# Kernel tuning notes

Hardware: AMD Instinct MI355X
Metric: run time of the kernel (lower is better)

The kernel has to match this reference:

```python
import jax, jax.numpy as jnp
import numpy as np

NEG_BIG = -9e15  # matches torch's -9000000000000000.0 masked-fill value
ALPHA = 0.2      # LeakyReLU negative slope


def setup_inputs() -> dict:
    key = jax.random.key(0)
    k1, k2, k3, k4 = jax.random.split(key, 4)
    N, F_in, F_out = 8192, 128, 64
    h = jax.random.normal(k1, (N, F_in), dtype=jnp.float32)
    adj = jax.random.randint(k2, (N, N), 0, 2).astype(jnp.float32)
    # Glorot(gain=1.414)-scale params
    W = jax.random.normal(k3, (F_in, F_out), dtype=jnp.float32) * (1.414 * np.sqrt(2.0 / (F_in + F_out)))
    a = jax.random.normal(k4, (2 * F_out, 1), dtype=jnp.float32) * (1.414 * np.sqrt(2.0 / (2 * F_out + 1)))
    return {"h": h, "adj": adj, "W": W, "a": a}


def reference(h, adj, W, a):
    F_out = W.shape[1]
    Wh = h @ W                               # [N, F_out]
    Wh1 = Wh @ a[:F_out, :]                  # [N, 1]
    Wh2 = Wh @ a[F_out:, :]                  # [N, 1]
    e = jax.nn.leaky_relu(Wh1 + Wh2.T, negative_slope=ALPHA)  # [N, N]
    attention = jnp.where(adj > 0, e, NEG_BIG)
    attention = jax.nn.softmax(attention, axis=1)
    # dropout omitted (eval mode / p applied only in training)
    h_prime = attention @ Wh                 # [N, F_out]
    return jax.nn.elu(h_prime)               # concat=True -> ELU
```

## Files before the change

### kernel.cpp

```cpp
#include <hip/hip_runtime.h>
#include <hip/hip_bf16.h>

#define N 8192
#define FIN 128
#define FOUT 64
#define ALPHA 0.2f
#define LOG2E 1.44269504f
#define JPW (N / 8)

typedef __attribute__((ext_vector_type(8))) short short8;
typedef __attribute__((ext_vector_type(4))) float f32x4;

static __device__ __forceinline__ unsigned fkey(float x) {
    unsigned u = __float_as_uint(x);
    return (u >> 31) ? ~u : (u | 0x80000000u);
}
static __device__ __forceinline__ float fdecode(unsigned k) {
    unsigned u = (k & 0x80000000u) ? (k & 0x7FFFFFFFu) : ~k;
    return __uint_as_float(u);
}

__global__ __launch_bounds__(256) void k_prep(const float* __restrict__ h,
                                              const float* __restrict__ W,
                                              const float* __restrict__ a,
                                              float* __restrict__ Wh,
                                              float* __restrict__ s,
                                              float* __restrict__ t,
                                              unsigned* __restrict__ keys) {
    __shared__ float lH[16 * FIN];
    __shared__ float lW[FIN * FOUT];
    __shared__ float red[8];
    const int tid = threadIdx.x;
    const int r0 = blockIdx.x * 16;
    {
        const float4* src = (const float4*)(h + (size_t)r0 * FIN);
        float4* dst = (float4*)lH;
        for (int i = tid; i < 16 * FIN / 4; i += 256) dst[i] = src[i];
        const float4* ws_ = (const float4*)W;
        float4* dw = (float4*)lW;
        for (int i = tid; i < FIN * FOUT / 4; i += 256) dw[i] = ws_[i];
    }
    __syncthreads();
    const int wave = tid >> 6, lane = tid & 63;
    float acc[4] = {0.f, 0.f, 0.f, 0.f};
    for (int k = 0; k < FIN; ++k) {
        float wv = lW[k * FOUT + lane];
#pragma unroll
        for (int r = 0; r < 4; ++r)
            acc[r] = fmaf(lH[(wave * 4 + r) * FIN + k], wv, acc[r]);
    }
    const float a1 = a[lane], a2 = a[FOUT + lane];
    float smx = -1e30f, tmx = -1e30f;
#pragma unroll
    for (int r = 0; r < 4; ++r) {
        int row = r0 + wave * 4 + r;
        Wh[(size_t)row * FOUT + lane] = acc[r];
        float sv = acc[r] * a1, tv = acc[r] * a2;
#pragma unroll
        for (int off = 32; off; off >>= 1) {
            sv += __shfl_xor(sv, off);
            tv += __shfl_xor(tv, off);
        }
        if (lane == 0) { s[row] = sv; t[row] = tv; }
        smx = fmaxf(smx, sv);
        tmx = fmaxf(tmx, tv);
    }
    if (lane == 0) { red[wave] = smx; red[4 + wave] = tmx; }
    __syncthreads();
    if (tid == 0) {
        float ms = fmaxf(fmaxf(red[0], red[1]), fmaxf(red[2], red[3]));
        float mt = fmaxf(fmaxf(red[4], red[5]), fmaxf(red[6], red[7]));
        atomicMax(keys + 0, fkey(ms));
        atomicMax(keys + 1, fkey(mt));
    }
}

__global__ __launch_bounds__(256) void k_pack(const float* __restrict__ Wh,
                                              __hip_bfloat16* __restrict__ WhB) {
    const int c = blockIdx.x;
    const int tn = threadIdx.x >> 6;
    const int lane = threadIdx.x & 63;
    const int quad = lane >> 4, l16 = lane & 15;
    const float* src = Wh + ((size_t)(c * 32 + quad * 8)) * FOUT + tn * 16 + l16;
    union { unsigned short u[8]; short8 v; } frag;
#pragma unroll
    for (int e = 0; e < 8; ++e) {
        __hip_bfloat16 b = __float2bfloat16(src[(size_t)e * FOUT]);
        frag.u[e] = *(unsigned short*)&b;
    }
    *(short8*)&WhB[(((size_t)c * 4 + tn) * 64 + lane) * 8] = frag.v;
}

__global__ __launch_bounds__(512, 4) void k_attn(const float* __restrict__ adj,
                                                 const __hip_bfloat16* __restrict__ WhB,
                                                 const float* __restrict__ s,
                                                 const float* __restrict__ t,
                                                 const unsigned* __restrict__ keys,
                                                 float* __restrict__ out) {
    __shared__ float shacc[8][4][64][4];
    __shared__ float shl[8][16];
    const int wave = threadIdx.x >> 6, lane = threadIdx.x & 63;
    const int quad = lane >> 4, l16 = lane & 15;
    const int i0 = blockIdx.x * 16;

    const float mraw = fdecode(keys[0]) + fdecode(keys[1]);
    const float mle = mraw > 0.f ? mraw : ALPHA * mraw;
    const float mm = mle * LOG2E;
    const float sm = s[i0 + l16];

    const float* arow = adj + (size_t)(i0 + l16) * N + wave * JPW + quad * 8;
    const float* trow = t + wave * JPW + quad * 8;
    const short8* BF = (const short8*)WhB;

    f32x4 acc0 = {0,0,0,0}, acc1 = {0,0,0,0}, acc2 = {0,0,0,0}, acc3 = {0,0,0,0};
    float lsum = 0.f;

    float4 ca0, ca1, ct0, ct1, na0, na1, nt0, nt1;
    ca0 = *(const float4*)(arow);     ca1 = *(const float4*)(arow + 4);
    ct0 = *(const float4*)(trow);     ct1 = *(const float4*)(trow + 4);

    const int UNITS = JPW / 32;
#pragma unroll 4
    for (int u = 0; u < UNITS; ++u) {
        if (u + 1 < UNITS) {
            const float* an = arow + (u + 1) * 32;
            const float* tn_ = trow + (u + 1) * 32;
            na0 = *(const float4*)(an);      na1 = *(const float4*)(an + 4);
            nt0 = *(const float4*)(tn_);     nt1 = *(const float4*)(tn_ + 4);
        }
        const size_t cidx = (size_t)(wave * UNITS + u) * 4;
        short8 b0 = BF[(cidx + 0) * 64 + lane];
        short8 b1 = BF[(cidx + 1) * 64 + lane];
        short8 b2 = BF[(cidx + 2) * 64 + lane];
        short8 b3 = BF[(cidx + 3) * 64 + lane];

        union { unsigned short u16[8]; short8 v; } af;
        const float* ap = (const float*)&ca0;
        const float* tp = (const float*)&ct0;
#pragma unroll
        for (int e = 0; e < 8; ++e) {
            float av = (e < 4) ? ap[e] : ((const float*)&ca1)[e - 4];
            float tv = (e < 4) ? tp[e] : ((const float*)&ct1)[e - 4];
            float x = sm + tv;
            float le = fmaxf(x, ALPHA * x);
            float ex = exp2f(fmaf(le, LOG2E, -mm));
            float p = av * ex;
            __hip_bfloat16 pb = __float2bfloat16(p);
            unsigned short ub = *(unsigned short*)&pb;
            af.u16[e] = ub;
            lsum += __uint_as_float(((unsigned)ub) << 16);
        }
        ca0 = na0; ca1 = na1; ct0 = nt0; ct1 = nt1;

        acc0 = __builtin_amdgcn_mfma_f32_16x16x32_bf16(af.v, b0, acc0, 0, 0, 0);
        acc1 = __builtin_amdgcn_mfma_f32_16x16x32_bf16(af.v, b1, acc1, 0, 0, 0);
        acc2 = __builtin_amdgcn_mfma_f32_16x16x32_bf16(af.v, b2, acc2, 0, 0, 0);
        acc3 = __builtin_amdgcn_mfma_f32_16x16x32_bf16(af.v, b3, acc3, 0, 0, 0);
    }

    lsum += __shfl_xor(lsum, 16);
    lsum += __shfl_xor(lsum, 32);

#pragma unroll
    for (int r = 0; r < 4; ++r) {
        shacc[wave][0][lane][r] = acc0[r];
        shacc[wave][1][lane][r] = acc1[r];
        shacc[wave][2][lane][r] = acc2[r];
        shacc[wave][3][lane][r] = acc3[r];
    }
    if (lane < 16) shl[wave][lane] = lsum;
    __syncthreads();

    if (wave == 4 && lane < 16) {
        float v = 0.f;
#pragma unroll
        for (int w = 0; w < 8; ++w) v += shl[w][lane];
        shl[0][lane] = v;
    }
    float tot[4] = {0.f, 0.f, 0.f, 0.f};
    if (wave < 4) {
#pragma unroll
        for (int w = 0; w < 8; ++w) {
            float4 c = *(const float4*)&shacc[w][wave][lane][0];
#pragma unroll
            for (int r = 0; r < 4; ++r) tot[r] += ((const float*)&c)[r];
        }
    }
    __syncthreads();
    if (wave < 4) {
#pragma unroll
        for (int r = 0; r < 4; ++r) {
            int row = quad * 4 + r;
            float l = shl[0][row];
            float v = tot[r] / l;
            float o = v > 0.f ? v : (exp2f(v * LOG2E) - 1.f);
            out[(size_t)(i0 + row) * FOUT + wave * 16 + l16] = o;
        }
    }
}

extern "C" void kernel_launch(void* const* d_in, const int* in_sizes, int n_in,
                              void* d_out, int out_size, void* d_ws, size_t ws_size,
                              hipStream_t stream) {
    const float* h   = (const float*)d_in[0];
    const float* adj = (const float*)d_in[1];
    const float* W   = (const float*)d_in[2];
    const float* a   = (const float*)d_in[3];
    float* out = (float*)d_out;

    float* Wh = (float*)d_ws;
    __hip_bfloat16* WhB = (__hip_bfloat16*)(Wh + (size_t)N * FOUT);
    float* s = (float*)(WhB + (size_t)N * FOUT);
    float* t = s + N;
    unsigned* keys = (unsigned*)(t + N);

    hipMemsetAsync(keys, 0, 2 * sizeof(unsigned), stream);
    k_prep<<<N / 16, 256, 0, stream>>>(h, W, a, Wh, s, t, keys);
    k_pack<<<N / 32, 256, 0, stream>>>(Wh, WhB);
    k_attn<<<N / 16, 512, 0, stream>>>(adj, WhB, s, t, keys, out);
}
```

Measured before the change: 427.1 us.

## Stage adjacency tiles through LDS with async global-to-LDS double buffering

Restructures the attention kernel so the block streams 256-column slabs of the adjacency rows and t into double-buffered LDS via global_load_lds, with a barrier per stage. Waves are now split into 4 output-column tiles by 2 column halves, so each wave keeps one MFMA accumulator instead of four, and the final cross-wave reduction shrinks. The exp/leaky-relu work is now repeated by the four column-tile waves (4x redundant transcendental work per element) in exchange for coalesced, asynchronous loads and lower register pressure. The occupancy hint in launch bounds is dropped and a barrier is added per stage.

```diff
diff --git a/kernel.cpp b/kernel.cpp
--- a/kernel.cpp
+++ b/kernel.cpp
@@ -6,7 +6,9 @@
 #define FOUT 64
 #define ALPHA 0.2f
 #define LOG2E 1.44269504f
-#define JPW (N / 8)
+#define STJ 256
+#define NSTAGES (N / STJ)
+#define RS 260
 
 typedef __attribute__((ext_vector_type(8))) short short8;
 typedef __attribute__((ext_vector_type(4))) float f32x4;
@@ -18,6 +20,12 @@
 static __device__ __forceinline__ float fdecode(unsigned k) {
     unsigned u = (k & 0x80000000u) ? (k & 0x7FFFFFFFu) : ~k;
     return __uint_as_float(u);
+}
+
+static __device__ __forceinline__ void gll16(const float* g, float* l) {
+    __builtin_amdgcn_global_load_lds(
+        (const __attribute__((address_space(1))) unsigned int*)g,
+        (__attribute__((address_space(3))) unsigned int*)l, 16, 0, 0);
 }
 
 __global__ __launch_bounds__(256) void k_prep(const float* __restrict__ h,
@@ -91,108 +99,94 @@
     *(short8*)&WhB[(((size_t)c * 4 + tn) * 64 + lane) * 8] = frag.v;
 }
 
-__global__ __launch_bounds__(512, 4) void k_attn(const float* __restrict__ adj,
-                                                 const __hip_bfloat16* __restrict__ WhB,
-                                                 const float* __restrict__ s,
-                                                 const float* __restrict__ t,
-                                                 const unsigned* __restrict__ keys,
-                                                 float* __restrict__ out) {
-    __shared__ float shacc[8][4][64][4];
-    __shared__ float shl[8][16];
+__global__ __launch_bounds__(512) void k_attn(const float* __restrict__ adj,
+                                              const __hip_bfloat16* __restrict__ WhB,
+                                              const float* __restrict__ s,
+                                              const float* __restrict__ t,
+                                              const unsigned* __restrict__ keys,
+                                              float* __restrict__ out) {
+    __shared__ float bufA[2][16 * RS];
+    __shared__ float bufT[2][STJ];
+    __shared__ float shacc[8][64][4];
+    __shared__ float shl[2][16];
     const int wave = threadIdx.x >> 6, lane = threadIdx.x & 63;
     const int quad = lane >> 4, l16 = lane & 15;
+    const int ct = wave & 3, jh = wave >> 2;
     const int i0 = blockIdx.x * 16;
 
     const float mraw = fdecode(keys[0]) + fdecode(keys[1]);
     const float mle = mraw > 0.f ? mraw : ALPHA * mraw;
     const float mm = mle * LOG2E;
     const float sm = s[i0 + l16];
-
-    const float* arow = adj + (size_t)(i0 + l16) * N + wave * JPW + quad * 8;
-    const float* trow = t + wave * JPW + quad * 8;
     const short8* BF = (const short8*)WhB;
 
-    f32x4 acc0 = {0,0,0,0}, acc1 = {0,0,0,0}, acc2 = {0,0,0,0}, acc3 = {0,0,0,0};
+    f32x4 acc = {0, 0, 0, 0};
     float lsum = 0.f;
 
-    float4 ca0, ca1, ct0, ct1, na0, na1, nt0, nt1;
-    ca0 = *(const float4*)(arow);     ca1 = *(const float4*)(arow + 4);
-    ct0 = *(const float4*)(trow);     ct1 = *(const float4*)(trow + 4);
-
-    const int UNITS = JPW / 32;
-#pragma unroll 4
-    for (int u = 0; u < UNITS; ++u) {
-        if (u + 1 < UNITS) {
-            const float* an = arow + (u + 1) * 32;
-            const float* tn_ = trow + (u + 1) * 32;
-            na0 = *(const float4*)(an);      na1 = *(const float4*)(an + 4);
-            nt0 = *(const float4*)(tn_);     nt1 = *(const float4*)(tn_ + 4);
-        }
-        const size_t cidx = (size_t)(wave * UNITS + u) * 4;
-        short8 b0 = BF[(cidx + 0) * 64 + lane];
-        short8 b1 = BF[(cidx + 1) * 64 + lane];
-        short8 b2 = BF[(cidx + 2) * 64 + lane];
-        short8 b3 = BF[(cidx + 3) * 64 + lane];
-
-        union { unsigned short u16[8]; short8 v; } af;
-        const float* ap = (const float*)&ca0;
-        const float* tp = (const float*)&ct0;
-#pragma unroll
-        for (int e = 0; e < 8; ++e) {
-            float av = (e < 4) ? ap[e] : ((const float*)&ca1)[e - 4];
-            float tv = (e < 4) ? tp[e] : ((const float*)&ct1)[e - 4];
-            float x = sm + tv;
-            float le = fmaxf(x, ALPHA * x);
-            float ex = exp2f(fmaf(le, LOG2E, -mm));
-            float p = av * ex;
-            __hip_bfloat16 pb = __float2bfloat16(p);
-            unsigned short ub = *(unsigned short*)&pb;
-            af.u16[e] = ub;
-            lsum += __uint_as_float(((unsigned)ub) << 16);
-        }
-        ca0 = na0; ca1 = na1; ct0 = nt0; ct1 = nt1;
-
-        acc0 = __builtin_amdgcn_mfma_f32_16x16x32_bf16(af.v, b0, acc0, 0, 0, 0);
-        acc1 = __builtin_amdgcn_mfma_f32_16x16x32_bf16(af.v, b1, acc1, 0, 0, 0);
-        acc2 = __builtin_amdgcn_mfma_f32_16x16x32_bf16(af.v, b2, acc2, 0, 0, 0);
-        acc3 = __builtin_amdgcn_mfma_f32_16x16x32_bf16(af.v, b3, acc3, 0, 0, 0);
+    const int r2 = 2 * wave;
+    const float* gadj = adj + (size_t)(i0 + r2) * N + lane * 4;
+
+    gll16(gadj, &bufA[0][r2 * RS]);
+    gll16(gadj + N, &bufA[0][(r2 + 1) * RS]);
+    if (wave == 0) gll16(t + lane * 4, &bufT[0][0]);
+    __syncthreads();
+
+    for (int st = 0; st < NSTAGES; ++st) {
+        const int b = st & 1;
+        if (st + 1 < NSTAGES) {
+            const float* g = gadj + (size_t)(st + 1) * STJ;
+            gll16(g, &bufA[b ^ 1][r2 * RS]);
+            gll16(g + N, &bufA[b ^ 1][(r2 + 1) * RS]);
+            if (wave == 0) gll16(t + (size_t)(st + 1) * STJ + lane * 4, &bufT[b ^ 1][0]);
+        }
+        const float* A = &bufA[b][0];
+        const float* T = &bufT[b][0];
+        const int cbase = st * 8 + jh * 4;
+        short8 Bf0 = BF[((cbase + 0) * 4 + ct) * 64 + lane];
+        short8 Bf1 = BF[((cbase + 1) * 4 + ct) * 64 + lane];
+        short8 Bf2 = BF[((cbase + 2) * 4 + ct) * 64 + lane];
+        short8 Bf3 = BF[((cbase + 3) * 4 + ct) * 64 + lane];
+#pragma unroll
+        for (int u = 0; u < 4; ++u) {
+            const int j0 = jh * 128 + u * 32 + quad * 8;
+            float4 a0 = *(const float4*)&A[l16 * RS + j0];
+            float4 a1 = *(const float4*)&A[l16 * RS + j0 + 4];
+            float4 t0 = *(const float4*)&T[j0];
+            float4 t1 = *(const float4*)&T[j0 + 4];
+            union { unsigned short u16[8]; short8 v; } af;
+#pragma unroll
+            for (int e = 0; e < 8; ++e) {
+                float av = (e < 4) ? ((const float*)&a0)[e] : ((const float*)&a1)[e - 4];
+                float tv = (e < 4) ? ((const float*)&t0)[e] : ((const float*)&t1)[e - 4];
+                float x = sm + tv;
+                float le = fmaxf(x, ALPHA * x);
+                float ex = exp2f(fmaf(le, LOG2E, -mm));
+                float p = av * ex;
+                __hip_bfloat16 pb = __float2bfloat16(p);
+                unsigned short ub = *(unsigned short*)&pb;
+                af.u16[e] = ub;
+                lsum += __uint_as_float(((unsigned)ub) << 16);
+            }
+            const short8 bb = (u == 0) ? Bf0 : (u == 1) ? Bf1 : (u == 2) ? Bf2 : Bf3;
+            acc = __builtin_amdgcn_mfma_f32_16x16x32_bf16(af.v, bb, acc, 0, 0, 0);
+        }
+        __syncthreads();
     }
 
     lsum += __shfl_xor(lsum, 16);
     lsum += __shfl_xor(lsum, 32);
-
-#pragma unroll
-    for (int r = 0; r < 4; ++r) {
-        shacc[wave][0][lane][r] = acc0[r];
-        shacc[wave][1][lane][r] = acc1[r];
-        shacc[wave][2][lane][r] = acc2[r];
-        shacc[wave][3][lane][r] = acc3[r];
-    }
-    if (lane < 16) shl[wave][lane] = lsum;
-    __syncthreads();
-
-    if (wave == 4 && lane < 16) {
-        float v = 0.f;
-#pragma unroll
-        for (int w = 0; w < 8; ++w) v += shl[w][lane];
-        shl[0][lane] = v;
-    }
-    float tot[4] = {0.f, 0.f, 0.f, 0.f};
+#pragma unroll
+    for (int r = 0; r < 4; ++r) shacc[wave][lane][r] = acc[r];
+    if (ct == 0 && lane < 16) shl[jh][lane] = lsum;
+    __syncthreads();
+
     if (wave < 4) {
 #pragma unroll
-        for (int w = 0; w < 8; ++w) {
-            float4 c = *(const float4*)&shacc[w][wave][lane][0];
-#pragma unroll
-            for (int r = 0; r < 4; ++r) tot[r] += ((const float*)&c)[r];
-        }
-    }
-    __syncthreads();
-    if (wave < 4) {
-#pragma unroll
         for (int r = 0; r < 4; ++r) {
+            float tot = shacc[wave][lane][r] + shacc[wave + 4][lane][r];
             int row = quad * 4 + r;
-            float l = shl[0][row];
-            float v = tot[r] / l;
+            float l = shl[0][row] + shl[1][row];
+            float v = tot / l;
             float o = v > 0.f ? v : (exp2f(v * LOG2E) - 1.f);
             out[(size_t)(i0 + row) * FOUT + wave * 16 + l16] = o;
         }
```

Measured after the change: 429.6 us. About the same (+0.6%).
